# Kernel optimization log

Measured on AMD Instinct MI355X. Metric: run time of the kernel, lower is better.

The kernel has to match this reference:

```python
import jax, jax.numpy as jnp
import numpy as np

EMB_DIM = 256
NUM_RELATIONS = 128
BATCH = 4096
LOG_SQRT_2PI = 0.9189385332046727  # 0.5*log(2*pi)


def setup_inputs() -> dict:
    key = jax.random.key(0)
    k1, k2, k3, k4, k5 = jax.random.split(key, 5)
    sbjs = jax.random.normal(k1, (BATCH, EMB_DIM), dtype=jnp.float32)
    objs = jax.random.normal(k2, (BATCH, EMB_DIM), dtype=jnp.float32)
    mus = jax.random.normal(k3, (NUM_RELATIONS, 2 * EMB_DIM), dtype=jnp.float32)
    sigmas = jnp.abs(jax.random.normal(k4, (NUM_RELATIONS, 2 * EMB_DIM), dtype=jnp.float32)) + 1.0
    relation_priors = jax.random.normal(k5, (NUM_RELATIONS,), dtype=jnp.float32)
    return {"sbjs": sbjs, "objs": objs, "mus": mus, "sigmas": sigmas,
            "relation_priors": relation_priors}


def reference(sbjs, objs, mus, sigmas, relation_priors):
    # x: [B, 2D] concatenated subject/object embeddings
    x = jnp.concatenate([sbjs, objs], axis=1)
    two_d = x.shape[1]
    # Gaussian log-pdf, broadcast over relations: [B, R, 2D]
    z = (x[:, None, :] - mus[None, :, :]) / sigmas[None, :, :]
    logp = -0.5 * z * z - jnp.log(sigmas)[None, :, :] - LOG_SQRT_2PI
    # Original adds prior to every one of the 2D dims before the sum,
    # so the prior contributes prior * 2D to each [b, r] output.
    return logp.sum(axis=-1) + relation_priors[None, :] * two_d
```

## Files before the change

### kernel.cpp

```cpp
#include <hip/hip_runtime.h>
#include <hip/hip_bf16.h>
#include <cstddef>
#include <cstdint>

#define EMB   256
#define TWOD  512
#define NREL  128
#define BATCH 4096
#define LOG_SQRT_2PI 0.9189385332046727f

typedef __bf16          bf16x8  __attribute__((ext_vector_type(8)));
typedef unsigned short  u16x8   __attribute__((ext_vector_type(8)));
typedef float           f32x4   __attribute__((ext_vector_type(4)));

__device__ __forceinline__ unsigned short f2bf(float f) {
    unsigned u = __builtin_bit_cast(unsigned, f);
    u = (u + 0x7FFFu + ((u >> 16) & 1u)) >> 16;
    return (unsigned short)u;
}

__device__ __forceinline__ bf16x8 pack8(float4 a, float4 b) {
    u16x8 u;
    u[0] = f2bf(a.x); u[1] = f2bf(a.y); u[2] = f2bf(a.z); u[3] = f2bf(a.w);
    u[4] = f2bf(b.x); u[5] = f2bf(b.y); u[6] = f2bf(b.z); u[7] = f2bf(b.w);
    return __builtin_bit_cast(bf16x8, u);
}

__global__ __launch_bounds__(64) void nb_prep(
    const float* __restrict__ mus, const float* __restrict__ sigmas,
    const float* __restrict__ priors,
    unsigned short* __restrict__ Wi, float* __restrict__ cst)
{
    const int r  = blockIdx.x;
    const int k8 = threadIdx.x;
    const float* mp = mus    + (size_t)r * TWOD + k8 * 8;
    const float* sp = sigmas + (size_t)r * TWOD + k8 * 8;
    const float4 m0 = *(const float4*)mp,       m1 = *(const float4*)(mp + 4);
    const float4 s0 = *(const float4*)sp,       s1 = *(const float4*)(sp + 4);

    float mu[8] = {m0.x, m0.y, m0.z, m0.w, m1.x, m1.y, m1.z, m1.w};
    float sg[8] = {s0.x, s0.y, s0.z, s0.w, s1.x, s1.y, s1.z, s1.w};

    u16x8 pc, pa;
    float esum = 0.0f;
    #pragma unroll
    for (int i = 0; i < 8; i++) {
        const float inv2 = 1.0f / (sg[i] * sg[i]);
        pc[i] = f2bf(mu[i] * inv2);
        pa[i] = f2bf(-0.5f * inv2);
        esum += -0.5f * mu[i] * mu[i] * inv2 - __logf(sg[i]) - LOG_SQRT_2PI;
    }
    unsigned short* w = Wi + (size_t)k8 * (NREL * 16) + r * 16;
    *(u16x8*)w       = pc;
    *(u16x8*)(w + 8) = pa;

    #pragma unroll
    for (int off = 32; off >= 1; off >>= 1)
        esum += __shfl_down(esum, off, 64);
    if (k8 == 0) cst[r] = esum + priors[r] * (float)TWOD;
}

__global__ __launch_bounds__(256, 1) void nb_fused(
    const float* __restrict__ sbjs, const float* __restrict__ objs,
    const unsigned short* __restrict__ Wi,
    const float* __restrict__ cst, float* __restrict__ out)
{
    const int tid  = threadIdx.x;
    const int wv   = tid >> 6;
    const int lane = tid & 63;
    const int m16  = lane & 15;
    const int quad = lane >> 4;
    const int b0   = blockIdx.x * 16;
    const int row  = b0 + m16;

    bf16x8 ax[16], ax2[16];
    #pragma unroll
    for (int fi = 0; fi < 16; fi++) {
        const int col = fi * 32 + quad * 8;
        const float* p = (col < EMB)
            ? (sbjs + (size_t)row * EMB + col)
            : (objs + (size_t)row * EMB + (col - EMB));
        const float4 v0 = *(const float4*)p;
        const float4 v1 = *(const float4*)(p + 4);
        ax[fi] = pack8(v0, v1);
        const float4 q0 = {v0.x * v0.x, v0.y * v0.y, v0.z * v0.z, v0.w * v0.w};
        const float4 q1 = {v1.x * v1.x, v1.y * v1.y, v1.z * v1.z, v1.w * v1.w};
        ax2[fi] = pack8(q0, q1);
    }

    f32x4 accc[2], acca[2];
    accc[0] = (f32x4)0.0f; accc[1] = (f32x4)0.0f;
    acca[0] = (f32x4)0.0f; acca[1] = (f32x4)0.0f;

    const unsigned short* wbase = Wi + (size_t)quad * (NREL * 16)
                                     + (wv * 32 + m16) * 16;
    #pragma unroll
    for (int fi = 0; fi < 16; fi++) {
        const unsigned short* wp = wbase + (size_t)fi * 4 * (NREL * 16);
        const bf16x8 bc0 = *(const bf16x8*)(wp);
        const bf16x8 ba0 = *(const bf16x8*)(wp + 8);
        const bf16x8 bc1 = *(const bf16x8*)(wp + 256);
        const bf16x8 ba1 = *(const bf16x8*)(wp + 264);
        accc[0] = __builtin_amdgcn_mfma_f32_16x16x32_bf16(ax [fi], bc0, accc[0], 0, 0, 0);
        acca[0] = __builtin_amdgcn_mfma_f32_16x16x32_bf16(ax2[fi], ba0, acca[0], 0, 0, 0);
        accc[1] = __builtin_amdgcn_mfma_f32_16x16x32_bf16(ax [fi], bc1, accc[1], 0, 0, 0);
        acca[1] = __builtin_amdgcn_mfma_f32_16x16x32_bf16(ax2[fi], ba1, acca[1], 0, 0, 0);
    }

    #pragma unroll
    for (int nt = 0; nt < 2; nt++) {
        const int r = wv * 32 + nt * 16 + m16;
        const float ca = cst[r];
        #pragma unroll
        for (int reg = 0; reg < 4; reg++)
            out[(size_t)(b0 + quad * 4 + reg) * NREL + r] =
                accc[nt][reg] + acca[nt][reg] + ca;
    }
}

__global__ __launch_bounds__(256) void nb_slow(
    const float* __restrict__ sbjs, const float* __restrict__ objs,
    const float* __restrict__ mus, const float* __restrict__ sigmas,
    const float* __restrict__ priors, float* __restrict__ out)
{
    const int idx = blockIdx.x * 256 + threadIdx.x;
    const int b = idx >> 7;
    const int r = idx & (NREL - 1);
    float acc = priors[r] * (float)TWOD;
    for (int k = 0; k < TWOD; k++) {
        const float x  = (k < EMB) ? sbjs[(size_t)b * EMB + k]
                                   : objs[(size_t)b * EMB + (k - EMB)];
        const float mu = mus[r * TWOD + k];
        const float s  = sigmas[r * TWOD + k];
        const float z  = (x - mu) / s;
        acc += -0.5f * z * z - logf(s) - LOG_SQRT_2PI;
    }
    out[idx] = acc;
}

extern "C" void kernel_launch(void* const* d_in, const int* in_sizes, int n_in,
                              void* d_out, int out_size, void* d_ws, size_t ws_size,
                              hipStream_t stream)
{
    const float* sbjs   = (const float*)d_in[0];
    const float* objs   = (const float*)d_in[1];
    const float* mus    = (const float*)d_in[2];
    const float* sigmas = (const float*)d_in[3];
    const float* priors = (const float*)d_in[4];
    float* out = (float*)d_out;

    char* ws = (char*)d_ws;
    const size_t o_w   = 0;
    const size_t o_cst = 256 << 10;
    const size_t need  = o_cst + NREL * sizeof(float);

    if (ws_size >= need) {
        unsigned short* Wi = (unsigned short*)(ws + o_w);
        float* cst = (float*)(ws + o_cst);
        nb_prep<<<NREL, 64, 0, stream>>>(mus, sigmas, priors, Wi, cst);
        nb_fused<<<BATCH / 16, 256, 0, stream>>>(sbjs, objs, Wi, cst, out);
    } else {
        nb_slow<<<(BATCH * NREL) / 256, 256, 0, stream>>>(
            sbjs, objs, mus, sigmas, priors, out);
    }
}
```

Baseline: 72.29 us.

## Fuse parameter prep into main kernel with per-block LDS weight staging

Merges the prep kernel and the MFMA kernel into one launch. Each of 256 blocks covers 32 relations and 64 batch rows. It recomputes the bf16 mu/sigma-derived weights for its relation slice into 64KB of shared memory, then reads them from LDS instead of a global workspace. This removes a kernel launch and the global round-trip, but the prep work is now done redundantly across 64 batch blocks per relation group. It also drops the workspace fallback path.

```diff
diff --git a/kernel.cpp b/kernel.cpp
--- a/kernel.cpp
+++ b/kernel.cpp
@@ -1,5 +1,4 @@
 #include <hip/hip_runtime.h>
-#include <hip/hip_bf16.h>
 #include <cstddef>
 #include <cstdint>
 
@@ -26,51 +25,57 @@
     return __builtin_bit_cast(bf16x8, u);
 }
 
-__global__ __launch_bounds__(64) void nb_prep(
-    const float* __restrict__ mus, const float* __restrict__ sigmas,
-    const float* __restrict__ priors,
-    unsigned short* __restrict__ Wi, float* __restrict__ cst)
+__global__ __launch_bounds__(256, 1) void nb_one(
+    const float* __restrict__ sbjs, const float* __restrict__ objs,
+    const float* __restrict__ mus,  const float* __restrict__ sigmas,
+    const float* __restrict__ priors, float* __restrict__ out)
 {
-    const int r  = blockIdx.x;
-    const int k8 = threadIdx.x;
-    const float* mp = mus    + (size_t)r * TWOD + k8 * 8;
-    const float* sp = sigmas + (size_t)r * TWOD + k8 * 8;
-    const float4 m0 = *(const float4*)mp,       m1 = *(const float4*)(mp + 4);
-    const float4 s0 = *(const float4*)sp,       s1 = *(const float4*)(sp + 4);
+    extern __shared__ unsigned short Wl[];
+    __shared__ float cstl[32];
 
-    float mu[8] = {m0.x, m0.y, m0.z, m0.w, m1.x, m1.y, m1.z, m1.w};
-    float sg[8] = {s0.x, s0.y, s0.z, s0.w, s1.x, s1.y, s1.z, s1.w};
+    const int tid = threadIdx.x;
+    const int rb  = blockIdx.x & 63;
+    const int rg  = blockIdx.x >> 6;
 
-    u16x8 pc, pa;
-    float esum = 0.0f;
-    #pragma unroll
-    for (int i = 0; i < 8; i++) {
-        const float inv2 = 1.0f / (sg[i] * sg[i]);
-        pc[i] = f2bf(mu[i] * inv2);
-        pa[i] = f2bf(-0.5f * inv2);
-        esum += -0.5f * mu[i] * mu[i] * inv2 - __logf(sg[i]) - LOG_SQRT_2PI;
+    {
+        const int rl = tid >> 3;
+        const int j0 = tid & 7;
+        const int R  = rg * 32 + rl;
+        const float* mp = mus    + (size_t)R * TWOD;
+        const float* sp = sigmas + (size_t)R * TWOD;
+        float esum = 0.0f;
+        #pragma unroll
+        for (int j = 0; j < 8; j++) {
+            const int k8 = j * 8 + j0;
+            const float4 m0 = *(const float4*)(mp + k8 * 8);
+            const float4 m1 = *(const float4*)(mp + k8 * 8 + 4);
+            const float4 s0 = *(const float4*)(sp + k8 * 8);
+            const float4 s1 = *(const float4*)(sp + k8 * 8 + 4);
+            const float mu[8] = {m0.x, m0.y, m0.z, m0.w, m1.x, m1.y, m1.z, m1.w};
+            const float sg[8] = {s0.x, s0.y, s0.z, s0.w, s1.x, s1.y, s1.z, s1.w};
+            u16x8 pc, pa;
+            #pragma unroll
+            for (int i = 0; i < 8; i++) {
+                const float inv2 = 1.0f / (sg[i] * sg[i]);
+                pc[i] = f2bf(mu[i] * inv2);
+                pa[i] = f2bf(-0.5f * inv2);
+                esum += -0.5f * mu[i] * mu[i] * inv2 - __logf(sg[i]) - LOG_SQRT_2PI;
+            }
+            unsigned short* w = Wl + k8 * 512 + rl * 8;
+            *(u16x8*)(w)       = pc;
+            *(u16x8*)(w + 256) = pa;
+        }
+        esum += __shfl_down(esum, 4, 64);
+        esum += __shfl_down(esum, 2, 64);
+        esum += __shfl_down(esum, 1, 64);
+        if (j0 == 0) cstl[rl] = esum + priors[R] * (float)TWOD;
     }
-    unsigned short* w = Wi + (size_t)k8 * (NREL * 16) + r * 16;
-    *(u16x8*)w       = pc;
-    *(u16x8*)(w + 8) = pa;
 
-    #pragma unroll
-    for (int off = 32; off >= 1; off >>= 1)
-        esum += __shfl_down(esum, off, 64);
-    if (k8 == 0) cst[r] = esum + priors[r] * (float)TWOD;
-}
-
-__global__ __launch_bounds__(256, 1) void nb_fused(
-    const float* __restrict__ sbjs, const float* __restrict__ objs,
-    const unsigned short* __restrict__ Wi,
-    const float* __restrict__ cst, float* __restrict__ out)
-{
-    const int tid  = threadIdx.x;
     const int wv   = tid >> 6;
     const int lane = tid & 63;
     const int m16  = lane & 15;
     const int quad = lane >> 4;
-    const int b0   = blockIdx.x * 16;
+    const int b0   = rb * 64 + wv * 16;
     const int row  = b0 + m16;
 
     bf16x8 ax[16], ax2[16];
@@ -88,19 +93,20 @@
         ax2[fi] = pack8(q0, q1);
     }
 
+    __syncthreads();
+
     f32x4 accc[2], acca[2];
     accc[0] = (f32x4)0.0f; accc[1] = (f32x4)0.0f;
     acca[0] = (f32x4)0.0f; acca[1] = (f32x4)0.0f;
 
-    const unsigned short* wbase = Wi + (size_t)quad * (NREL * 16)
-                                     + (wv * 32 + m16) * 16;
+    const unsigned short* wbase = Wl + quad * 512 + m16 * 8;
     #pragma unroll
     for (int fi = 0; fi < 16; fi++) {
-        const unsigned short* wp = wbase + (size_t)fi * 4 * (NREL * 16);
+        const unsigned short* wp = wbase + fi * 4 * 512;
         const bf16x8 bc0 = *(const bf16x8*)(wp);
-        const bf16x8 ba0 = *(const bf16x8*)(wp + 8);
-        const bf16x8 bc1 = *(const bf16x8*)(wp + 256);
-        const bf16x8 ba1 = *(const bf16x8*)(wp + 264);
+        const bf16x8 bc1 = *(const bf16x8*)(wp + 128);
+        const bf16x8 ba0 = *(const bf16x8*)(wp + 256);
+        const bf16x8 ba1 = *(const bf16x8*)(wp + 384);
         accc[0] = __builtin_amdgcn_mfma_f32_16x16x32_bf16(ax [fi], bc0, accc[0], 0, 0, 0);
         acca[0] = __builtin_amdgcn_mfma_f32_16x16x32_bf16(ax2[fi], ba0, acca[0], 0, 0, 0);
         accc[1] = __builtin_amdgcn_mfma_f32_16x16x32_bf16(ax [fi], bc1, accc[1], 0, 0, 0);
@@ -109,33 +115,14 @@
 
     #pragma unroll
     for (int nt = 0; nt < 2; nt++) {
-        const int r = wv * 32 + nt * 16 + m16;
-        const float ca = cst[r];
+        const int rl = nt * 16 + m16;
+        const int R  = rg * 32 + rl;
+        const float ca = cstl[rl];
         #pragma unroll
         for (int reg = 0; reg < 4; reg++)
-            out[(size_t)(b0 + quad * 4 + reg) * NREL + r] =
+            out[(size_t)(b0 + quad * 4 + reg) * NREL + R] =
                 accc[nt][reg] + acca[nt][reg] + ca;
     }
-}
-
-__global__ __launch_bounds__(256) void nb_slow(
-    const float* __restrict__ sbjs, const float* __restrict__ objs,
-    const float* __restrict__ mus, const float* __restrict__ sigmas,
-    const float* __restrict__ priors, float* __restrict__ out)
-{
-    const int idx = blockIdx.x * 256 + threadIdx.x;
-    const int b = idx >> 7;
-    const int r = idx & (NREL - 1);
-    float acc = priors[r] * (float)TWOD;
-    for (int k = 0; k < TWOD; k++) {
-        const float x  = (k < EMB) ? sbjs[(size_t)b * EMB + k]
-                                   : objs[(size_t)b * EMB + (k - EMB)];
-        const float mu = mus[r * TWOD + k];
-        const float s  = sigmas[r * TWOD + k];
-        const float z  = (x - mu) / s;
-        acc += -0.5f * z * z - logf(s) - LOG_SQRT_2PI;
-    }
-    out[idx] = acc;
 }
 
 extern "C" void kernel_launch(void* const* d_in, const int* in_sizes, int n_in,
@@ -149,18 +136,7 @@
     const float* priors = (const float*)d_in[4];
     float* out = (float*)d_out;
 
-    char* ws = (char*)d_ws;
-    const size_t o_w   = 0;
-    const size_t o_cst = 256 << 10;
-    const size_t need  = o_cst + NREL * sizeof(float);
+    (void)d_ws; (void)ws_size;
 
-    if (ws_size >= need) {
-        unsigned short* Wi = (unsigned short*)(ws + o_w);
-        float* cst = (float*)(ws + o_cst);
-        nb_prep<<<NREL, 64, 0, stream>>>(mus, sigmas, priors, Wi, cst);
-        nb_fused<<<BATCH / 16, 256, 0, stream>>>(sbjs, objs, Wi, cst, out);
-    } else {
-        nb_slow<<<(BATCH * NREL) / 256, 256, 0, stream>>>(
-            sbjs, objs, mus, sigmas, priors, out);
-    }
+    nb_one<<<256, 256, 64 << 10, stream>>>(sbjs, objs, mus, sigmas, priors, out);
 }
```

After: 75.86 us. 4.9% more time.
